# Kernel tuning notes

Measured on AMD Instinct MI355X. Metric: run time of the kernel, lower is better.

## Reference

```python
import jax, jax.numpy as jnp
import numpy as np

B, S, D, U, A = 8, 2048, 1024, 1024, 4  # batch, seq, input_dim, units, n_activations


def setup_inputs() -> dict:
    key = jax.random.key(0)
    ks = jax.random.split(key, 6)
    scale_w = (6.0 / (D + U)) ** 0.5  # glorot_uniform
    scale_wf = (6.0 / (U + A)) ** 0.5
    scale_wa = (6.0 / (D + A)) ** 0.5
    return {
        "x": jax.random.normal(ks[0], (B, S, D), dtype=jnp.float32),
        "w": jax.random.uniform(ks[1], (D, U), jnp.float32, -scale_w, scale_w),
        "b": jnp.zeros((U,), jnp.float32),
        "wf": jax.random.uniform(ks[2], (U, A), jnp.float32, -scale_wf, scale_wf),
        "bf": jnp.zeros((U, A), jnp.float32),
        "w_att": jax.random.uniform(ks[3], (D, A), jnp.float32, -scale_wa, scale_wa),
        "b_att": jnp.zeros((A,), jnp.float32),
    }


def reference(x, w, b, wf, bf, w_att, b_att):
    # weighted_sum: [B,S,U]
    ws = jnp.einsum('bsd,du->bsu', x, w) + b
    # broadcast per-activation affine: [B,S,U,A]
    wa = ws[..., None] * wf + bf
    acts = [
        jax.nn.relu(wa[..., 0]),
        jax.nn.sigmoid(wa[..., 1]),
        jnp.tanh(wa[..., 2]),
        jax.nn.gelu(wa[..., 3], approximate=False),  # tf.nn.gelu default is exact
    ]
    result_activations = jnp.stack(acts, axis=-1)  # [B,S,U,A]
    # attention over activations: [B,S,A]
    attn = jax.nn.softmax(jnp.einsum('bsd,da->bsa', x, w_att) + b_att, axis=-1)
    # weighted reduce over activation axis -> [B,S,U]
    out = jnp.einsum('bsua,bsa->bsu', result_activations, attn)
    return out
```

## Files before the change

### kernel.cpp

```cpp
#include <hip/hip_runtime.h>
#include <hip/hip_bf16.h>
#include <cstdint>

#define B_ 8
#define S_ 2048
#define D_ 1024
#define U_ 1024
#define M_ (B_ * S_)

typedef __bf16 bf16x8 __attribute__((ext_vector_type(8)));
typedef float  f32x4  __attribute__((ext_vector_type(4)));

__device__ __forceinline__ uint16_t f2bf(float f) {
  uint32_t u = __builtin_bit_cast(uint32_t, f);
  u += 0x7fffu + ((u >> 16) & 1u);
  return (uint16_t)(u >> 16);
}

__device__ __forceinline__ void async_copy16(const void* g, void* l) {
  typedef const __attribute__((address_space(1))) uint8_t* gp_t;
  typedef __attribute__((address_space(3))) uint8_t* lp_t;
  __builtin_amdgcn_global_load_lds((gp_t)(uintptr_t)g,
                                   (lp_t)(uint32_t)(uintptr_t)l, 16, 0, 0);
}

__global__ __launch_bounds__(256) void k_prep(
    const float* __restrict__ x, const float* __restrict__ w_att,
    const float* __restrict__ b_att, const float* __restrict__ w,
    uint16_t* __restrict__ x_bf, float* __restrict__ attn,
    uint16_t* __restrict__ wt) {
  __shared__ float tile[32][33];
  const int bid = blockIdx.x;
  if (bid < M_ / 4) {
    const int wave = threadIdx.x >> 6, lane = threadIdx.x & 63;
    const int row = bid * 4 + wave;
    const float4* xr = reinterpret_cast<const float4*>(x + (size_t)row * D_);
    const float4* wa4 = reinterpret_cast<const float4*>(w_att);
    float4 v[4];
#pragma unroll
    for (int i = 0; i < 4; i++) v[i] = xr[lane + 64 * i];
    float4 p = {0.f, 0.f, 0.f, 0.f};
#pragma unroll
    for (int i = 0; i < 4; i++) {
      const int base = 4 * (lane + 64 * i);
      const float xe[4] = {v[i].x, v[i].y, v[i].z, v[i].w};
#pragma unroll
      for (int c = 0; c < 4; c++) {
        float4 wv = wa4[base + c];
        p.x = fmaf(xe[c], wv.x, p.x);
        p.y = fmaf(xe[c], wv.y, p.y);
        p.z = fmaf(xe[c], wv.z, p.z);
        p.w = fmaf(xe[c], wv.w, p.w);
      }
      ushort4 hb;
      hb.x = f2bf(v[i].x); hb.y = f2bf(v[i].y);
      hb.z = f2bf(v[i].z); hb.w = f2bf(v[i].w);
      reinterpret_cast<ushort4*>(x_bf + (size_t)row * D_)[lane + 64 * i] = hb;
    }
#pragma unroll
    for (int off = 32; off > 0; off >>= 1) {
      p.x += __shfl_xor(p.x, off);
      p.y += __shfl_xor(p.y, off);
      p.z += __shfl_xor(p.z, off);
      p.w += __shfl_xor(p.w, off);
    }
    if (lane == 0) {
      float l0 = p.x + b_att[0], l1 = p.y + b_att[1];
      float l2 = p.z + b_att[2], l3 = p.w + b_att[3];
      float mx = fmaxf(fmaxf(l0, l1), fmaxf(l2, l3));
      float e0 = __expf(l0 - mx), e1 = __expf(l1 - mx);
      float e2 = __expf(l2 - mx), e3 = __expf(l3 - mx);
      float inv = __builtin_amdgcn_rcpf(e0 + e1 + e2 + e3);
      reinterpret_cast<float4*>(attn)[row] =
          make_float4(e0 * inv, e1 * inv, e2 * inv, e3 * inv);
    }
  } else {
    const int wid = bid - M_ / 4;
    const int t = threadIdx.x;
    const int tx = t & 31, ty = t >> 5;
    const int c0 = (wid & 31) * 32;
    const int r0 = (wid >> 5) * 32;
#pragma unroll
    for (int i = 0; i < 4; i++) {
      int r = ty + i * 8;
      tile[r][tx] = w[(size_t)(r0 + r) * U_ + c0 + tx];
    }
    __syncthreads();
#pragma unroll
    for (int i = 0; i < 4; i++) {
      int r = ty + i * 8;
      wt[(size_t)(c0 + r) * D_ + r0 + tx] = f2bf(tile[tx][r]);
    }
  }
}

#define BM 128
#define BN 128
#define BK 64

__global__ __launch_bounds__(256, 4) void k_gemm_ep(
    const uint16_t* __restrict__ xbf, const uint16_t* __restrict__ wt,
    const float* __restrict__ bias, const float* __restrict__ wf,
    const float* __restrict__ bfb, const float* __restrict__ attn,
    float* __restrict__ out) {
  __shared__ uint16_t As[BM * BK];
  __shared__ uint16_t Bs[BN * BK];

  const int t = threadIdx.x;
  const int wave = t >> 6, lane = t & 63;
  const int l16 = lane & 15, quad = lane >> 4;
  const int wm = wave >> 1, wn = wave & 1;
  const int m0 = blockIdx.y * BM;
  const int n0 = blockIdx.x * BN;

  const uint16_t* aBase = xbf + (size_t)m0 * D_;
  const uint16_t* bBase = wt + (size_t)n0 * D_;

  f32x4 acc[4][4] = {};

  for (int k0 = 0; k0 < D_; k0 += BK) {
#pragma unroll
    for (int it = 0; it < 4; it++) {
      int c = t + it * 256;
      int r = c >> 3;
      int cs = c & 7;
      int gc = cs ^ (r & 7);
      async_copy16(aBase + (size_t)r * D_ + k0 + gc * 8, (uint8_t*)As + c * 16);
      async_copy16(bBase + (size_t)r * D_ + k0 + gc * 8, (uint8_t*)Bs + c * 16);
    }
    __syncthreads();

#pragma unroll
    for (int ks = 0; ks < 2; ks++) {
      const int kcb = ks * 4;
      bf16x8 af[4], bfr[4];
#pragma unroll
      for (int i = 0; i < 4; i++) {
        int r = wm * 64 + i * 16 + l16;
        int cs = (kcb + quad) ^ (r & 7);
        af[i] = *reinterpret_cast<const bf16x8*>(&As[r * BK + cs * 8]);
      }
#pragma unroll
      for (int j = 0; j < 4; j++) {
        int n = wn * 64 + j * 16 + l16;
        int cs = (kcb + quad) ^ (n & 7);
        bfr[j] = *reinterpret_cast<const bf16x8*>(&Bs[n * BK + cs * 8]);
      }
#pragma unroll
      for (int i = 0; i < 4; i++)
#pragma unroll
        for (int j = 0; j < 4; j++)
          acc[i][j] = __builtin_amdgcn_mfma_f32_16x16x32_bf16(af[i], bfr[j], acc[i][j], 0, 0, 0);
    }
    __syncthreads();
  }

  float bu[4];
  float4 wf4[4], bf4[4];
#pragma unroll
  for (int j = 0; j < 4; j++) {
    int u = n0 + wn * 64 + j * 16 + l16;
    bu[j] = bias[u];
    wf4[j] = reinterpret_cast<const float4*>(wf)[u];
    bf4[j] = reinterpret_cast<const float4*>(bfb)[u];
  }
#pragma unroll
  for (int i = 0; i < 4; i++) {
#pragma unroll
    for (int r = 0; r < 4; r++) {
      int mg = m0 + wm * 64 + i * 16 + quad * 4 + r;
      float4 at = reinterpret_cast<const float4*>(attn)[mg];
      float* orow = out + (size_t)mg * U_;
#pragma unroll
      for (int j = 0; j < 4; j++) {
        int u = n0 + wn * 64 + j * 16 + l16;
        float wsv = acc[i][j][r] + bu[j];
        float wa0 = fmaf(wsv, wf4[j].x, bf4[j].x);
        float wa1 = fmaf(wsv, wf4[j].y, bf4[j].y);
        float wa2 = fmaf(wsv, wf4[j].z, bf4[j].z);
        float wa3 = fmaf(wsv, wf4[j].w, bf4[j].w);
        float a_relu = fmaxf(wa0, 0.f);
        float a_sig = __builtin_amdgcn_rcpf(
            1.f + __builtin_amdgcn_exp2f(-1.4426950409f * wa1));
        float a_tanh = fmaf(2.f, __builtin_amdgcn_rcpf(
            1.f + __builtin_amdgcn_exp2f(-2.8853900818f * wa2)), -1.f);
        float y = wa3 * fmaf(0.044715f, wa3 * wa3, 1.f);
        float a_gelu = wa3 * __builtin_amdgcn_rcpf(
            1.f + __builtin_amdgcn_exp2f(-2.302207929f * y));
        orow[u] = at.x * a_relu + at.y * a_sig + at.z * a_tanh + at.w * a_gelu;
      }
    }
  }
}

extern "C" void kernel_launch(void* const* d_in, const int* in_sizes, int n_in,
                              void* d_out, int out_size, void* d_ws, size_t ws_size,
                              hipStream_t stream) {
  const float* x     = (const float*)d_in[0];
  const float* w     = (const float*)d_in[1];
  const float* b     = (const float*)d_in[2];
  const float* wf    = (const float*)d_in[3];
  const float* bfb   = (const float*)d_in[4];
  const float* w_att = (const float*)d_in[5];
  const float* b_att = (const float*)d_in[6];
  float* out = (float*)d_out;

  char* ws = (char*)d_ws;
  uint16_t* x_bf = (uint16_t*)ws;
  uint16_t* w_t  = (uint16_t*)(ws + ((size_t)32 << 20));
  float*    attn = (float*)(ws + ((size_t)34 << 20));

  k_prep<<<dim3(M_ / 4 + 1024), 256, 0, stream>>>(x, w_att, b_att, w, x_bf, attn, w_t);
  k_gemm_ep<<<dim3(U_ / BN, M_ / BM), 256, 0, stream>>>(x_bf, w_t, b, wf, bfb, attn, out);
}
```

Baseline: 179.5 us.

## Use 256x256 tiles with double-buffered 8-phase pipelined MFMA GEMM and block swizzle

Grows the GEMM tile to 256x256 with 512 threads and double-buffers the LDS tiles. The main loop is split into eight phases, each issuing async global-to-LDS copies for upcoming K slices while MFMAs run on the current buffer, with explicit vmcnt waits, barriers and setprio. Workgroup indices are remapped so that nearby blocks share A and B tiles in cache. The aim is to hide load latency and raise arithmetic intensity. The cost is heavier register and LDS use (128 KB of LDS per block) and fewer resident blocks, with only 256 blocks in the grid.

```diff
diff --git a/kernel.cpp b/kernel.cpp
--- a/kernel.cpp
+++ b/kernel.cpp
@@ -94,100 +94,164 @@
   }
 }
 
-#define BM 128
-#define BN 128
+#define BM 256
+#define BN 256
 #define BK 64
-
-__global__ __launch_bounds__(256, 4) void k_gemm_ep(
+#define NKT (D_ / BK)
+
+__global__ __launch_bounds__(512, 2) void k_gemm_ep(
     const uint16_t* __restrict__ xbf, const uint16_t* __restrict__ wt,
     const float* __restrict__ bias, const float* __restrict__ wf,
     const float* __restrict__ bfb, const float* __restrict__ attn,
     float* __restrict__ out) {
-  __shared__ uint16_t As[BM * BK];
-  __shared__ uint16_t Bs[BN * BK];
+  __shared__ uint16_t As[2][BM * BK];
+  __shared__ uint16_t Bs[2][BN * BK];
 
   const int t = threadIdx.x;
-  const int wave = t >> 6, lane = t & 63;
+  const int lane = t & 63;
+  const int wave = t >> 6;
   const int l16 = lane & 15, quad = lane >> 4;
-  const int wm = wave >> 1, wn = wave & 1;
-  const int m0 = blockIdx.y * BM;
-  const int n0 = blockIdx.x * BN;
+  const int wm = wave >> 2;
+  const int wn = wave & 3;
+
+  const int h = blockIdx.y * (U_ / BN) + blockIdx.x;
+  const int l = (h & 7) * 32 + (h >> 3);
+  const int bx = l & 3;
+  const int by = l >> 2;
+  const int m0 = by * BM;
+  const int n0 = bx * BN;
 
   const uint16_t* aBase = xbf + (size_t)m0 * D_;
   const uint16_t* bBase = wt + (size_t)n0 * D_;
 
-  f32x4 acc[4][4] = {};
-
-  for (int k0 = 0; k0 < D_; k0 += BK) {
-#pragma unroll
-    for (int it = 0; it < 4; it++) {
-      int c = t + it * 256;
-      int r = c >> 3;
-      int cs = c & 7;
-      int gc = cs ^ (r & 7);
-      async_copy16(aBase + (size_t)r * D_ + k0 + gc * 8, (uint8_t*)As + c * 16);
-      async_copy16(bBase + (size_t)r * D_ + k0 + gc * 8, (uint8_t*)Bs + c * 16);
-    }
-    __syncthreads();
-
-#pragma unroll
-    for (int ks = 0; ks < 2; ks++) {
-      const int kcb = ks * 4;
-      bf16x8 af[4], bfr[4];
-#pragma unroll
-      for (int i = 0; i < 4; i++) {
-        int r = wm * 64 + i * 16 + l16;
-        int cs = (kcb + quad) ^ (r & 7);
-        af[i] = *reinterpret_cast<const bf16x8*>(&As[r * BK + cs * 8]);
-      }
-#pragma unroll
-      for (int j = 0; j < 4; j++) {
-        int n = wn * 64 + j * 16 + l16;
-        int cs = (kcb + quad) ^ (n & 7);
-        bfr[j] = *reinterpret_cast<const bf16x8*>(&Bs[n * BK + cs * 8]);
-      }
-#pragma unroll
-      for (int i = 0; i < 4; i++)
-#pragma unroll
-        for (int j = 0; j < 4; j++)
-          acc[i][j] = __builtin_amdgcn_mfma_f32_16x16x32_bf16(af[i], bfr[j], acc[i][j], 0, 0, 0);
-    }
-    __syncthreads();
+  f32x4 acc[2][2][4][2] = {};
+
+#define STAGE_A(BF, H, KS) do {                                              \
+    const uint16_t* _g = aBase + (size_t)((H) * 128) * D_ + (KS) * BK;       \
+    uint8_t* _l = (uint8_t*)As + (BF) * (BM * BK * 2) + (H) * 128 * BK * 2;  \
+    int _c0 = t;                                                             \
+    async_copy16(_g + (size_t)(_c0 >> 3) * D_ + ((_c0 & 7) ^ ((_c0 >> 3) & 7)) * 8, \
+                 _l + _c0 * 16);                                             \
+    int _c1 = t + 512;                                                       \
+    async_copy16(_g + (size_t)(_c1 >> 3) * D_ + ((_c1 & 7) ^ ((_c1 >> 3) & 7)) * 8, \
+                 _l + _c1 * 16);                                             \
+  } while (0)
+
+#define STAGE_B(BF, H, KS) do {                                              \
+    const uint16_t* _g = bBase + (size_t)((H) * 128) * D_ + (KS) * BK;       \
+    uint8_t* _l = (uint8_t*)Bs + (BF) * (BN * BK * 2) + (H) * 128 * BK * 2;  \
+    int _c0 = t;                                                             \
+    async_copy16(_g + (size_t)(_c0 >> 3) * D_ + ((_c0 & 7) ^ ((_c0 >> 3) & 7)) * 8, \
+                 _l + _c0 * 16);                                             \
+    int _c1 = t + 512;                                                       \
+    async_copy16(_g + (size_t)(_c1 >> 3) * D_ + ((_c1 & 7) ^ ((_c1 >> 3) & 7)) * 8, \
+                 _l + _c1 * 16);                                             \
+  } while (0)
+
+#define VM4 asm volatile("s_waitcnt vmcnt(4)" ::: "memory")
+#define NOWAIT
+
+#define PHASE(BF, MH, NH, STAGE, WAIT) do {                                  \
+    __builtin_amdgcn_sched_barrier(0);                  \
+    bf16x8 _a[4][2], _b[2][2];                                               \
+    _Pragma("unroll")                                                        \
+    for (int i = 0; i < 4; i++) {                                            \
+      int r = (MH) * 128 + wm * 64 + i * 16 + l16;                           \
+      _Pragma("unroll")                                                      \
+      for (int kh = 0; kh < 2; kh++) {                                       \
+        int cs = (kh * 4 + quad) ^ (r & 7);                                  \
+        _a[i][kh] = *reinterpret_cast<const bf16x8*>(&As[BF][r * BK + cs * 8]); \
+      }                                                                      \
+    }                                                                        \
+    _Pragma("unroll")                                                        \
+    for (int j = 0; j < 2; j++) {                                            \
+      int n = (NH) * 128 + wn * 32 + j * 16 + l16;                           \
+      _Pragma("unroll")                                                      \
+      for (int kh = 0; kh < 2; kh++) {                                       \
+        int cs = (kh * 4 + quad) ^ (n & 7);                                  \
+        _b[j][kh] = *reinterpret_cast<const bf16x8*>(&Bs[BF][n * BK + cs * 8]); \
+      }                                                                      \
+    }                                                                        \
+    STAGE;                                                                   \
+    __builtin_amdgcn_sched_barrier(0);  \
+    __builtin_amdgcn_s_barrier();                                            \
+    asm volatile("s_waitcnt lgkmcnt(0)" ::: "memory");                       \
+    __builtin_amdgcn_sched_barrier(0);           \
+    __builtin_amdgcn_s_setprio(1);                                           \
+    _Pragma("unroll")                                                        \
+    for (int kh = 0; kh < 2; kh++)                                           \
+      _Pragma("unroll")                                                      \
+      for (int i = 0; i < 4; i++)                                            \
+        _Pragma("unroll")                                                    \
+        for (int j = 0; j < 2; j++)                                          \
+          acc[MH][NH][i][j] = __builtin_amdgcn_mfma_f32_16x16x32_bf16(       \
+              _a[i][kh], _b[j][kh], acc[MH][NH][i][j], 0, 0, 0);             \
+    __builtin_amdgcn_s_setprio(0);                                           \
+    WAIT;                                                                    \
+    __builtin_amdgcn_s_barrier();                                            \
+  } while (0)
+
+  STAGE_A(0, 0, 0); STAGE_B(0, 0, 0); STAGE_A(0, 1, 0); STAGE_B(0, 1, 0);
+  STAGE_A(1, 0, 1); STAGE_B(1, 0, 1);
+  asm volatile("s_waitcnt vmcnt(4)" ::: "memory");
+  __builtin_amdgcn_s_barrier();
+
+  for (int it = 0; it < 8; ++it) {
+    const int t1k = 2 * it + 1;
+    const int s0 = (2 * it + 2 < NKT) ? 2 * it + 2 : NKT - 1;
+    const int s1 = (2 * it + 3 < NKT) ? 2 * it + 3 : NKT - 1;
+
+    PHASE(0, 0, 0, STAGE_B(1, 1, t1k), NOWAIT);
+    PHASE(0, 0, 1, STAGE_A(1, 1, t1k), NOWAIT);
+    PHASE(0, 1, 0, STAGE_A(0, 0, s0),  NOWAIT);
+    PHASE(0, 1, 1, STAGE_B(0, 0, s0),  VM4);
+    PHASE(1, 0, 0, STAGE_A(0, 1, s0),  NOWAIT);
+    PHASE(1, 0, 1, STAGE_B(0, 1, s0),  NOWAIT);
+    PHASE(1, 1, 0, STAGE_A(1, 0, s1),  NOWAIT);
+    PHASE(1, 1, 1, STAGE_B(1, 0, s1),  VM4);
   }
 
-  float bu[4];
-  float4 wf4[4], bf4[4];
-#pragma unroll
-  for (int j = 0; j < 4; j++) {
-    int u = n0 + wn * 64 + j * 16 + l16;
-    bu[j] = bias[u];
-    wf4[j] = reinterpret_cast<const float4*>(wf)[u];
-    bf4[j] = reinterpret_cast<const float4*>(bfb)[u];
-  }
-#pragma unroll
-  for (int i = 0; i < 4; i++) {
-#pragma unroll
-    for (int r = 0; r < 4; r++) {
-      int mg = m0 + wm * 64 + i * 16 + quad * 4 + r;
-      float4 at = reinterpret_cast<const float4*>(attn)[mg];
-      float* orow = out + (size_t)mg * U_;
-#pragma unroll
-      for (int j = 0; j < 4; j++) {
-        int u = n0 + wn * 64 + j * 16 + l16;
-        float wsv = acc[i][j][r] + bu[j];
-        float wa0 = fmaf(wsv, wf4[j].x, bf4[j].x);
-        float wa1 = fmaf(wsv, wf4[j].y, bf4[j].y);
-        float wa2 = fmaf(wsv, wf4[j].z, bf4[j].z);
-        float wa3 = fmaf(wsv, wf4[j].w, bf4[j].w);
-        float a_relu = fmaxf(wa0, 0.f);
-        float a_sig = __builtin_amdgcn_rcpf(
-            1.f + __builtin_amdgcn_exp2f(-1.4426950409f * wa1));
-        float a_tanh = fmaf(2.f, __builtin_amdgcn_rcpf(
-            1.f + __builtin_amdgcn_exp2f(-2.8853900818f * wa2)), -1.f);
-        float y = wa3 * fmaf(0.044715f, wa3 * wa3, 1.f);
-        float a_gelu = wa3 * __builtin_amdgcn_rcpf(
-            1.f + __builtin_amdgcn_exp2f(-2.302207929f * y));
-        orow[u] = at.x * a_relu + at.y * a_sig + at.z * a_tanh + at.w * a_gelu;
+  float  bu[2][2];
+  float4 wfv[2][2], bfv[2][2];
+#pragma unroll
+  for (int NH = 0; NH < 2; NH++)
+#pragma unroll
+    for (int j = 0; j < 2; j++) {
+      int u = n0 + NH * 128 + wn * 32 + j * 16 + l16;
+      bu[NH][j]  = bias[u];
+      wfv[NH][j] = reinterpret_cast<const float4*>(wf)[u];
+      bfv[NH][j] = reinterpret_cast<const float4*>(bfb)[u];
+    }
+#pragma unroll
+  for (int MH = 0; MH < 2; MH++) {
+#pragma unroll
+    for (int i = 0; i < 4; i++) {
+#pragma unroll
+      for (int r = 0; r < 4; r++) {
+        int mg = m0 + MH * 128 + wm * 64 + i * 16 + quad * 4 + r;
+        float4 at = reinterpret_cast<const float4*>(attn)[mg];
+        float* orow = out + (size_t)mg * U_;
+#pragma unroll
+        for (int NH = 0; NH < 2; NH++) {
+#pragma unroll
+          for (int j = 0; j < 2; j++) {
+            int u = n0 + NH * 128 + wn * 32 + j * 16 + l16;
+            float wsv = acc[MH][NH][i][j][r] + bu[NH][j];
+            float wa0 = fmaf(wsv, wfv[NH][j].x, bfv[NH][j].x);
+            float wa1 = fmaf(wsv, wfv[NH][j].y, bfv[NH][j].y);
+            float wa2 = fmaf(wsv, wfv[NH][j].z, bfv[NH][j].z);
+            float wa3 = fmaf(wsv, wfv[NH][j].w, bfv[NH][j].w);
+            float a_relu = fmaxf(wa0, 0.f);
+            float a_sig = __builtin_amdgcn_rcpf(
+                1.f + __builtin_amdgcn_exp2f(-1.4426950409f * wa1));
+            float a_tanh = fmaf(2.f, __builtin_amdgcn_rcpf(
+                1.f + __builtin_amdgcn_exp2f(-2.8853900818f * wa2)), -1.f);
+            float y = wa3 * fmaf(0.044715f, wa3 * wa3, 1.f);
+            float a_gelu = wa3 * __builtin_amdgcn_rcpf(
+                1.f + __builtin_amdgcn_exp2f(-2.302207929f * y));
+            orow[u] = at.x * a_relu + at.y * a_sig + at.z * a_tanh + at.w * a_gelu;
+          }
+        }
       }
     }
   }
@@ -211,5 +275,5 @@
   float*    attn = (float*)(ws + ((size_t)34 << 20));
 
   k_prep<<<dim3(M_ / 4 + 1024), 256, 0, stream>>>(x, w_att, b_att, w, x_bf, attn, w_t);
-  k_gemm_ep<<<dim3(U_ / BN, M_ / BM), 256, 0, stream>>>(x_bf, w_t, b, wf, bfb, attn, out);
-}
+  k_gemm_ep<<<dim3(U_ / BN, M_ / BM), 512, 0, stream>>>(x_bf, w_t, b, wf, bfb, attn, out);
+}
```

Measured after the change: 173.5 us. 3.3% less time.
